# Kernel optimization log

Hardware: AMD Instinct MI355X
Metric: run time of the kernel (lower is better)

The kernel has to match this reference:

```python
import jax, jax.numpy as jnp
import numpy as np

N_NODES = 50000
N_EDGES = 800000
NUM_FEATURES = 3
HIDDEN = 128
NUM_GRAPHS = 100
NUM_CLASSES = 2


def setup_inputs() -> dict:
    key = jax.random.key(0)
    ks = jax.random.split(key, 12)
    x = jax.random.normal(ks[0], (N_NODES, NUM_FEATURES), dtype=jnp.float32)
    edge_index = jax.random.randint(ks[1], (2, N_EDGES), 0, N_NODES, dtype=jnp.int64)
    batch = jnp.sort(jax.random.randint(ks[2], (N_NODES,), 0, NUM_GRAPHS, dtype=jnp.int64))
    c1, c2, c3 = 4 * HIDDEN, 2 * HIDDEN, HIDDEN  # 512, 256, 128

    def glorot(k, fan_in, fan_out):
        s = jnp.sqrt(6.0 / (fan_in + fan_out)).astype(jnp.float32)
        return jax.random.uniform(k, (fan_in, fan_out), jnp.float32, -s, s)

    W1 = glorot(ks[3], NUM_FEATURES, c1); b1 = jnp.zeros((c1,), jnp.float32)
    W2 = glorot(ks[4], c1, c2);           b2 = jnp.zeros((c2,), jnp.float32)
    W3 = glorot(ks[5], c2, c3);           b3 = jnp.zeros((c3,), jnp.float32)
    Wc = glorot(ks[6], c3, NUM_CLASSES);  bc = jnp.zeros((NUM_CLASSES,), jnp.float32)
    return {"x": x, "W1": W1, "b1": b1, "W2": W2, "b2": b2, "W3": W3, "b3": b3,
            "Wc": Wc, "bc": bc, "edge_index": edge_index, "batch": batch}


def reference(x, W1, b1, W2, b2, W3, b3, Wc, bc, edge_index, batch):
    n = x.shape[0]
    self_loop = jnp.arange(n, dtype=edge_index.dtype)
    row = jnp.concatenate([edge_index[0], self_loop])  # source nodes (messages from)
    col = jnp.concatenate([edge_index[1], self_loop])  # target nodes (aggregate into)
    # symmetric GCN normalization with self-loops: deg^{-1/2}[row] * deg^{-1/2}[col]
    deg = jax.ops.segment_sum(jnp.ones(row.shape, x.dtype), col, num_segments=n)
    dis = jnp.where(deg > 0, jax.lax.rsqrt(jnp.maximum(deg, 1.0)), 0.0)
    norm = dis[row] * dis[col]  # [E + N]

    def gcn_conv(h, W, b):
        m = h @ W                                   # project first (cheap GEMM)
        agg = jax.ops.segment_sum(norm[:, None] * m[row], col, num_segments=n)
        return agg + b

    h = jax.nn.relu(gcn_conv(x, W1, b1))
    h = jax.nn.relu(gcn_conv(h, W2, b2))
    h = jax.nn.relu(gcn_conv(h, W3, b3))

    # global mean pool over graphs
    counts = jax.ops.segment_sum(jnp.ones((n,), h.dtype), batch, num_segments=NUM_GRAPHS)
    pooled = jax.ops.segment_sum(h, batch, num_segments=NUM_GRAPHS) / jnp.maximum(counts, 1.0)[:, None]

    logits = pooled @ Wc + bc
    return jax.nn.log_softmax(logits, axis=1)
```

## Files before the change

kernel.cpp:

```cpp
#include <hip/hip_runtime.h>
#include <hip/hip_bf16.h>
#include <hip/hip_fp8.h>
#include <math.h>

#define N_NODES 50000
#define N_EDGES 800000
#define NFEAT 3
#define C1 512
#define C2 256
#define C3 128
#define NGRAPH 100
#define NCLS 2
#define PSPLIT 8
#define NRANGE 8
#define RANGE_SZ 6250

typedef short bh8 __attribute__((ext_vector_type(8)));
typedef float f32x4 __attribute__((ext_vector_type(4)));

__device__ __forceinline__ short f2bf(float x) {
    __hip_bfloat16 h = __float2bfloat16(x);
    return *reinterpret_cast<short*>(&h);
}
__device__ __forceinline__ float bflo(unsigned int u) { return __uint_as_float(u << 16); }
__device__ __forceinline__ float bfhi(unsigned int u) { return __uint_as_float(u & 0xffff0000u); }
__device__ __forceinline__ unsigned int packbf(float a, float b) {
    return (unsigned int)(unsigned short)f2bf(a) | ((unsigned int)(unsigned short)f2bf(b) << 16);
}
__device__ __forceinline__ unsigned char f2fp8(float x) {
    __hip_fp8_e4m3 q(x);
    return (unsigned char)q.__x;
}
__device__ __forceinline__ float2 fp8x2(unsigned short u) {
    __hip_fp8x2_e4m3 q; q.__x = u; return (float2)q;
}


__global__ void count_edges(const int* __restrict__ col, int* __restrict__ counts) {
    int range = blockIdx.x & (NRANGE - 1);
    int e = (blockIdx.x >> 3) * 256 + threadIdx.x;
    if (e < N_EDGES) {
        int c = col[e];
        int lo = range * RANGE_SZ;
        if (c >= lo && c < lo + RANGE_SZ) atomicAdd(&counts[c], 1);
    }
}


__global__ void scan_chunks(const int* __restrict__ counts, const float* __restrict__ x,
                            int* __restrict__ offsets, int* __restrict__ chunksums,
                            float* __restrict__ dis, float4* __restrict__ xd) {
    __shared__ int s[256];
    int b = blockIdx.x, t = threadIdx.x;
    int i = b * 256 + t;
    int v = (i < N_NODES) ? counts[i] : 0;
    if (i < N_NODES) {
        float d = rsqrtf((float)(v + 1));
        dis[i] = d;
        xd[i] = make_float4(x[i * 3 + 0], x[i * 3 + 1], x[i * 3 + 2], d);
    }
    s[t] = v;
    __syncthreads();
    for (int d = 1; d < 256; d <<= 1) {
        int add = (t >= d) ? s[t - d] : 0;
        __syncthreads();
        s[t] += add;
        __syncthreads();
    }
    if (i < N_NODES) offsets[i + 1] = s[t];
    if (t == 255) chunksums[b] = s[255];
}

__global__ void scan_sums(int* __restrict__ chunksums, int nchunks) {
    __shared__ int s[256];
    int t = threadIdx.x;
    int v = (t < nchunks) ? chunksums[t] : 0;
    s[t] = v;
    __syncthreads();
    for (int d = 1; d < 256; d <<= 1) {
        int add = (t >= d) ? s[t - d] : 0;
        __syncthreads();
        s[t] += add;
        __syncthreads();
    }
    if (t < nchunks) chunksums[t] = (t == 0) ? 0 : s[t - 1];
}

__global__ void finalize_offsets(int* __restrict__ offsets, const int* __restrict__ chunkoffs,
                                 int* __restrict__ cursor) {
    int i = blockIdx.x * blockDim.x + threadIdx.x;
    if (i < N_NODES) {
        int v = offsets[i + 1] + chunkoffs[i / 256];
        offsets[i + 1] = v;
        if (i + 1 < N_NODES) cursor[i + 1] = v;
    }
    if (i == 0) { offsets[0] = 0; cursor[0] = 0; }
}

__global__ void scatter_edges(const int* __restrict__ rowi, const int* __restrict__ coli,
                              int* __restrict__ cursor, int* __restrict__ csr_src) {
    int range = blockIdx.x & (NRANGE - 1);
    int e = (blockIdx.x >> 3) * 256 + threadIdx.x;
    if (e < N_EDGES) {
        int c = coli[e];
        int lo = range * RANGE_SZ;
        if (c >= lo && c < lo + RANGE_SZ) {
            int p = atomicAdd(&cursor[c], 1);
            csr_src[p] = rowi[e];
        }
    }
}


__global__ void prep_weights(const float* __restrict__ W2, const float* __restrict__ W3,
                             short* __restrict__ W2t, short* __restrict__ W3t) {
    int idx = blockIdx.x * 256 + threadIdx.x;
    if (idx < C1 * C2) {
        int n = idx / C1, k = idx % C1;
        W2t[idx] = f2bf(W2[k * C2 + n]);
    } else if (idx < C1 * C2 + C2 * C3) {
        int j = idx - C1 * C2;
        int n = j / C2, k = j % C2;
        W3t[j] = f2bf(W3[k * C3 + n]);
    }
}


__global__ __launch_bounds__(256) void agg_feat3(const float4* __restrict__ xd,
                                                 const int* __restrict__ offsets,
                                                 const int* __restrict__ csr_src,
                                                 float* __restrict__ aggx) {
    int t = threadIdx.x;
    int l = t & 15;
    int i = blockIdx.x * 16 + (t >> 4);
    if (i >= N_NODES) return;
    int s = offsets[i], e = offsets[i + 1];
    float a0 = 0.f, a1 = 0.f, a2 = 0.f;
    for (int p = s + l; p < e; p += 16) {
        int r = csr_src[p];
        float4 v = xd[r];
        a0 += v.w * v.x;
        a1 += v.w * v.y;
        a2 += v.w * v.z;
    }
#pragma unroll
    for (int m = 1; m < 16; m <<= 1) {
        a0 += __shfl_xor(a0, m);
        a1 += __shfl_xor(a1, m);
        a2 += __shfl_xor(a2, m);
    }
    if (l == 0) {
        float4 self = xd[i];
        float di = self.w;
        a0 += di * self.x; a1 += di * self.y; a2 += di * self.z;
        aggx[i * 3 + 0] = di * a0;
        aggx[i * 3 + 1] = di * a1;
        aggx[i * 3 + 2] = di * a2;
    }
}


__global__ __launch_bounds__(512, 4) void gemm_l1(const float* __restrict__ aggx,
                                                  const float* __restrict__ W1,
                                                  const float* __restrict__ b1,
                                                  const float* __restrict__ dis,
                                                  const short* __restrict__ Bt,
                                                  unsigned char* __restrict__ Cmat, int M) {
    __shared__ short As[128 * 32];
    __shared__ short Bs[C2 * 32];
    __shared__ float sW1[3 * C1];
    __shared__ float sb1[C1];
    __shared__ float sa[128 * 3];
    __shared__ float sd[128];
    int bm = blockIdx.x * 128;
    int t = threadIdx.x;
    int wave = t >> 6, lane = t & 63, quad = lane >> 4, l16 = lane & 15;
    int wm = (wave >> 2) * 64;
    int wn = (wave & 3) * 64;
    f32x4 acc[4][4] = {};

    for (int j = t; j < 3 * C1; j += 512) sW1[j] = W1[j];
    if (t < C1) sb1[t] = b1[t];
    if (t < 128 * 3) {
        int r = bm + t / 3; if (r > M - 1) r = M - 1;
        sa[t] = aggx[r * 3 + (t % 3)];
    }
    if (t < 128) {
        int r = bm + t; if (r > M - 1) r = M - 1;
        sd[t] = dis[r];
    }
    __syncthreads();

    int ar = t >> 2, ak = (t & 3) * 8;
    int br = t >> 1, bk = (t & 1) * 16;
    float a0 = sa[ar * 3 + 0], a1 = sa[ar * 3 + 1], a2 = sa[ar * 3 + 2];
    float drow = sd[ar];

    for (int k0 = 0; k0 < C1; k0 += 32) {
#pragma unroll
        for (int j = 0; j < 8; ++j) {
            int k = k0 + ak + j;
            float v = a0 * sW1[k] + a1 * sW1[C1 + k] + a2 * sW1[2 * C1 + k] + sb1[k];
            As[ar * 32 + ak + j] = f2bf(drow * fmaxf(v, 0.f));
        }
        const short* bptr = Bt + (size_t)br * C1 + bk + k0;
        *(bh8*)&Bs[br * 32 + bk]     = *(const bh8*)bptr;
        *(bh8*)&Bs[br * 32 + bk + 8] = *(const bh8*)(bptr + 8);
        __syncthreads();
        bh8 af[4], bf[4];
#pragma unroll
        for (int mt = 0; mt < 4; ++mt)
            af[mt] = *(const bh8*)&As[(wm + mt * 16 + l16) * 32 + quad * 8];
#pragma unroll
        for (int nt = 0; nt < 4; ++nt)
            bf[nt] = *(const bh8*)&Bs[(wn + nt * 16 + l16) * 32 + quad * 8];
#pragma unroll
        for (int mt = 0; mt < 4; ++mt)
#pragma unroll
            for (int nt = 0; nt < 4; ++nt)
                acc[mt][nt] = __builtin_amdgcn_mfma_f32_16x16x32_bf16(af[mt], bf[nt], acc[mt][nt], 0, 0, 0);
        __syncthreads();
    }

#pragma unroll
    for (int mt = 0; mt < 4; ++mt)
#pragma unroll
        for (int nt = 0; nt < 4; ++nt) {
            int colc = wn + nt * 16 + l16;
#pragma unroll
            for (int r = 0; r < 4; ++r) {
                int rowc = bm + wm + mt * 16 + quad * 4 + r;
                if (rowc < M) Cmat[(size_t)rowc * C2 + colc] = f2fp8(acc[mt][nt][r]);
            }
        }
}


template <int K, int BN>
__global__ __launch_bounds__(512, 4) void gemm_bf16(const short* __restrict__ A,
                                                    const short* __restrict__ Bt,
                                                    unsigned char* __restrict__ Cmat, int M) {
    __shared__ short As[128 * 32];
    __shared__ short Bs[BN * 32];
    constexpr int NT = BN / 64;
    int bm = blockIdx.x * 128;
    int t = threadIdx.x;
    int wave = t >> 6, lane = t & 63, quad = lane >> 4, l16 = lane & 15;
    int wm = (wave >> 2) * 64;
    int wn = (wave & 3) * (BN / 4);
    f32x4 acc[4][NT] = {};

    int ar = t >> 2, ak = (t & 3) * 8;
    int agr = bm + ar; if (agr > M - 1) agr = M - 1;
    const short* aptr = A + (size_t)agr * K + ak;

    for (int k0 = 0; k0 < K; k0 += 32) {
        *(bh8*)&As[ar * 32 + ak] = *(const bh8*)(aptr + k0);
        if constexpr (BN == 256) {
            int br = t >> 1, bk = (t & 1) * 16;
            const short* bptr = Bt + (size_t)br * K + bk + k0;
            *(bh8*)&Bs[br * 32 + bk]     = *(const bh8*)bptr;
            *(bh8*)&Bs[br * 32 + bk + 8] = *(const bh8*)(bptr + 8);
        } else {
            int br = t >> 2, bk = (t & 3) * 8;
            *(bh8*)&Bs[br * 32 + bk] = *(const bh8*)(Bt + (size_t)br * K + bk + k0);
        }
        __syncthreads();
        bh8 af[4], bf[NT];
#pragma unroll
        for (int mt = 0; mt < 4; ++mt)
            af[mt] = *(const bh8*)&As[(wm + mt * 16 + l16) * 32 + quad * 8];
#pragma unroll
        for (int nt = 0; nt < NT; ++nt)
            bf[nt] = *(const bh8*)&Bs[(wn + nt * 16 + l16) * 32 + quad * 8];
#pragma unroll
        for (int mt = 0; mt < 4; ++mt)
#pragma unroll
            for (int nt = 0; nt < NT; ++nt)
                acc[mt][nt] = __builtin_amdgcn_mfma_f32_16x16x32_bf16(af[mt], bf[nt], acc[mt][nt], 0, 0, 0);
        __syncthreads();
    }

#pragma unroll
    for (int mt = 0; mt < 4; ++mt)
#pragma unroll
        for (int nt = 0; nt < NT; ++nt) {
            int colc = wn + nt * 16 + l16;
#pragma unroll
            for (int r = 0; r < 4; ++r) {
                int rowc = bm + wm + mt * 16 + quad * 4 + r;
                if (rowc < M) Cmat[(size_t)rowc * BN + colc] = f2fp8(acc[mt][nt][r]);
            }
        }
}


template <int C, bool PRESCALE>
__global__ void aggregate_ns(const unsigned char* __restrict__ m, const int* __restrict__ offsets,
                             const int* __restrict__ csr_src, const float* __restrict__ dis,
                             const float* __restrict__ bias, short* __restrict__ out) {
    int i = blockIdx.x;
    int t = threadIdx.x;
    float di = dis[i];
    const unsigned short* mu = (const unsigned short*)m;
    float2 sf = fp8x2(mu[(size_t)i * (C / 2) + t]);
    float acc0 = sf.x, acc1 = sf.y;
    int s = offsets[i], e = offsets[i + 1];
    int p = s;
    for (; p + 8 <= e; p += 8) {
        int r0 = csr_src[p],     r1 = csr_src[p + 1], r2 = csr_src[p + 2], r3 = csr_src[p + 3];
        int r4 = csr_src[p + 4], r5 = csr_src[p + 5], r6 = csr_src[p + 6], r7 = csr_src[p + 7];
        unsigned short u0 = mu[(size_t)r0 * (C / 2) + t];
        unsigned short u1 = mu[(size_t)r1 * (C / 2) + t];
        unsigned short u2 = mu[(size_t)r2 * (C / 2) + t];
        unsigned short u3 = mu[(size_t)r3 * (C / 2) + t];
        unsigned short u4 = mu[(size_t)r4 * (C / 2) + t];
        unsigned short u5 = mu[(size_t)r5 * (C / 2) + t];
        unsigned short u6 = mu[(size_t)r6 * (C / 2) + t];
        unsigned short u7 = mu[(size_t)r7 * (C / 2) + t];
        float2 f0 = fp8x2(u0), f1 = fp8x2(u1), f2 = fp8x2(u2), f3 = fp8x2(u3);
        float2 f4 = fp8x2(u4), f5 = fp8x2(u5), f6 = fp8x2(u6), f7 = fp8x2(u7);
        acc0 += f0.x + f1.x + f2.x + f3.x + f4.x + f5.x + f6.x + f7.x;
        acc1 += f0.y + f1.y + f2.y + f3.y + f4.y + f5.y + f6.y + f7.y;
    }
    for (; p < e; ++p) {
        int r = csr_src[p];
        float2 f = fp8x2(mu[(size_t)r * (C / 2) + t]);
        acc0 += f.x;
        acc1 += f.y;
    }
    acc0 = fmaxf(di * acc0 + bias[2 * t], 0.f);
    acc1 = fmaxf(di * acc1 + bias[2 * t + 1], 0.f);
    if (PRESCALE) { acc0 *= di; acc1 *= di; }
    ((unsigned int*)out)[(size_t)i * (C / 2) + t] = packbf(acc0, acc1);
}


__global__ void pool_partial(const short* __restrict__ h3, const int* __restrict__ batch,
                             float* __restrict__ pooled) {
    int g = blockIdx.x, sp = blockIdx.y;
    int t = threadIdx.x;
    __shared__ int seg[2];
    if (t < 2) {
        int target = g + t;
        int lo = 0, hi = N_NODES;
        while (lo < hi) { int mid = (lo + hi) >> 1; if (batch[mid] < target) lo = mid + 1; else hi = mid; }
        seg[t] = lo;
    }
    __syncthreads();
    int start = seg[0], end = seg[1];
    int len = end - start;
    int chunk = (len + PSPLIT - 1) / PSPLIT;
    int a = start + sp * chunk;
    int b = a + chunk; if (b > end) b = end;
    if (a >= b) return;
    const unsigned int* hu = (const unsigned int*)h3;
    float s0 = 0.f, s1 = 0.f;
    int i = a;
    for (; i + 4 <= b; i += 4) {
        unsigned int u0 = hu[(size_t)(i + 0) * (C3 / 2) + t];
        unsigned int u1 = hu[(size_t)(i + 1) * (C3 / 2) + t];
        unsigned int u2 = hu[(size_t)(i + 2) * (C3 / 2) + t];
        unsigned int u3 = hu[(size_t)(i + 3) * (C3 / 2) + t];
        s0 += bflo(u0) + bflo(u1) + bflo(u2) + bflo(u3);
        s1 += bfhi(u0) + bfhi(u1) + bfhi(u2) + bfhi(u3);
    }
    for (; i < b; ++i) {
        unsigned int u = hu[(size_t)i * (C3 / 2) + t];
        s0 += bflo(u);
        s1 += bfhi(u);
    }
    atomicAdd(&pooled[g * C3 + 2 * t], s0);
    atomicAdd(&pooled[g * C3 + 2 * t + 1], s1);
}


__global__ void finalize_head(const float* __restrict__ pooled, const int* __restrict__ batch,
                              const float* __restrict__ Wc, const float* __restrict__ bc,
                              float* __restrict__ outp) {
    int g = blockIdx.x;
    int t = threadIdx.x;
    __shared__ int seg[2];
    if (t < 2) {
        int target = g + t;
        int lo = 0, hi = N_NODES;
        while (lo < hi) { int mid = (lo + hi) >> 1; if (batch[mid] < target) lo = mid + 1; else hi = mid; }
        seg[t] = lo;
    }
    __syncthreads();
    float cnt = (float)(seg[1] - seg[0]);
    float pv = pooled[(size_t)g * C3 + t] / fmaxf(cnt, 1.f);
    float p0 = pv * Wc[t * 2 + 0];
    float p1 = pv * Wc[t * 2 + 1];
#pragma unroll
    for (int o = 32; o > 0; o >>= 1) {
        p0 += __shfl_down(p0, o);
        p1 += __shfl_down(p1, o);
    }
    __shared__ float r0[2], r1[2];
    int wid = t >> 6, lane = t & 63;
    if (lane == 0) { r0[wid] = p0; r1[wid] = p1; }
    __syncthreads();
    if (t == 0) {
        float l0 = r0[0] + r0[1] + bc[0];
        float l1 = r1[0] + r1[1] + bc[1];
        float mx = fmaxf(l0, l1);
        float lse = mx + logf(expf(l0 - mx) + expf(l1 - mx));
        outp[g * 2 + 0] = l0 - lse;
        outp[g * 2 + 1] = l1 - lse;
    }
}


extern "C" void kernel_launch(void* const* d_in, const int* in_sizes, int n_in,
                              void* d_out, int out_size, void* d_ws, size_t ws_size,
                              hipStream_t stream) {
    const float* x = (const float*)d_in[0];
    const float* W1 = (const float*)d_in[1];
    const float* b1 = (const float*)d_in[2];
    const float* W2 = (const float*)d_in[3];
    const float* b2 = (const float*)d_in[4];
    const float* W3 = (const float*)d_in[5];
    const float* b3 = (const float*)d_in[6];
    const float* Wc = (const float*)d_in[7];
    const float* bc = (const float*)d_in[8];
    const int* ei = (const int*)d_in[9];
    const int* batch = (const int*)d_in[10];
    const int* row = ei;
    const int* col = ei + N_EDGES;
    float* out = (float*)d_out;

    char* ws = (char*)d_ws;
    size_t off = 0;
    auto alloc = [&](size_t bytes) -> void* {
        off = (off + 255) & ~(size_t)255;
        void* p = ws + off;
        off += bytes;
        return p;
    };

    int* counts = (int*)alloc((size_t)N_NODES * 4);
    int* offsets = (int*)alloc((size_t)(N_NODES + 1) * 4);
    int* cursor = (int*)alloc((size_t)N_NODES * 4);
    int* chunksums = (int*)alloc(256 * 4);
    float* dis = (float*)alloc((size_t)N_NODES * 4);
    float4* xd = (float4*)alloc((size_t)N_NODES * 16);
    int* csr_src = (int*)alloc((size_t)N_EDGES * 4);
    float* aggx = (float*)alloc((size_t)N_NODES * 3 * 4);
    short* W2t = (short*)alloc((size_t)C1 * C2 * 2);
    short* W3t = (short*)alloc((size_t)C2 * C3 * 2);
    unsigned char* m2 = (unsigned char*)alloc((size_t)N_NODES * C2);
    short* h2 = (short*)alloc((size_t)N_NODES * C2 * 2);
    unsigned char* m3 = (unsigned char*)alloc((size_t)N_NODES * C3);
    short* h3 = (short*)alloc((size_t)N_NODES * C3 * 2);
    float* pooled = (float*)alloc((size_t)NGRAPH * C3 * 4);

    hipMemsetAsync(counts, 0, (size_t)N_NODES * 4, stream);
    hipMemsetAsync(pooled, 0, (size_t)NGRAPH * C3 * 4, stream);
    int nechunks = (N_EDGES + 255) / 256;
    count_edges<<<nechunks * NRANGE, 256, 0, stream>>>(col, counts);
    int nchunks = (N_NODES + 255) / 256;
    scan_chunks<<<nchunks, 256, 0, stream>>>(counts, x, offsets, chunksums, dis, xd);
    scan_sums<<<1, 256, 0, stream>>>(chunksums, nchunks);
    finalize_offsets<<<(N_NODES + 255) / 256, 256, 0, stream>>>(offsets, chunksums, cursor);
    scatter_edges<<<nechunks * NRANGE, 256, 0, stream>>>(row, col, cursor, csr_src);

    prep_weights<<<(C1 * C2 + C2 * C3 + 255) / 256, 256, 0, stream>>>(W2, W3, W2t, W3t);

    agg_feat3<<<(N_NODES + 15) / 16, 256, 0, stream>>>(xd, offsets, csr_src, aggx);

    gemm_l1<<<(N_NODES + 127) / 128, 512, 0, stream>>>(aggx, W1, b1, dis, W2t, m2, N_NODES);
    aggregate_ns<C2, true><<<N_NODES, C2 / 2, 0, stream>>>(m2, offsets, csr_src, dis, b2, h2);

    gemm_bf16<C2, C3><<<(N_NODES + 127) / 128, 512, 0, stream>>>(h2, W3t, m3, N_NODES);
    aggregate_ns<C3, false><<<N_NODES, C3 / 2, 0, stream>>>(m3, offsets, csr_src, dis, b3, h3);

    dim3 gp(NGRAPH, PSPLIT);
    pool_partial<<<gp, C3 / 2, 0, stream>>>(h3, batch, pooled);
    finalize_head<<<NGRAPH, C3, 0, stream>>>(pooled, batch, Wc, bc, out);
}
```

Baseline: 301.5 us.

## Aggregate with one wavefront per node, wider loads and deeper gather unroll

Replaces the per-node block aggregation with a kernel that packs four nodes per 256-thread block, one 64-lane wavefront per node. For C=256, each lane loads 4 fp8 values as a uint32. Node offsets and scale are made wave-uniform via readfirstlane, the gather is unrolled to 16 neighbours, and the tail is handled with a masked 16-wide batch. The aim is fewer tiny blocks, more memory-level parallelism per wave and wider loads. The cost is higher register pressure and some wasted tail loads.

```diff
diff --git a/kernel.cpp b/kernel.cpp
--- a/kernel.cpp
+++ b/kernel.cpp
@@ -296,43 +296,111 @@
 
 
 template <int C, bool PRESCALE>
-__global__ void aggregate_ns(const unsigned char* __restrict__ m, const int* __restrict__ offsets,
-                             const int* __restrict__ csr_src, const float* __restrict__ dis,
-                             const float* __restrict__ bias, short* __restrict__ out) {
-    int i = blockIdx.x;
-    int t = threadIdx.x;
-    float di = dis[i];
-    const unsigned short* mu = (const unsigned short*)m;
-    float2 sf = fp8x2(mu[(size_t)i * (C / 2) + t]);
-    float acc0 = sf.x, acc1 = sf.y;
-    int s = offsets[i], e = offsets[i + 1];
-    int p = s;
-    for (; p + 8 <= e; p += 8) {
-        int r0 = csr_src[p],     r1 = csr_src[p + 1], r2 = csr_src[p + 2], r3 = csr_src[p + 3];
-        int r4 = csr_src[p + 4], r5 = csr_src[p + 5], r6 = csr_src[p + 6], r7 = csr_src[p + 7];
-        unsigned short u0 = mu[(size_t)r0 * (C / 2) + t];
-        unsigned short u1 = mu[(size_t)r1 * (C / 2) + t];
-        unsigned short u2 = mu[(size_t)r2 * (C / 2) + t];
-        unsigned short u3 = mu[(size_t)r3 * (C / 2) + t];
-        unsigned short u4 = mu[(size_t)r4 * (C / 2) + t];
-        unsigned short u5 = mu[(size_t)r5 * (C / 2) + t];
-        unsigned short u6 = mu[(size_t)r6 * (C / 2) + t];
-        unsigned short u7 = mu[(size_t)r7 * (C / 2) + t];
-        float2 f0 = fp8x2(u0), f1 = fp8x2(u1), f2 = fp8x2(u2), f3 = fp8x2(u3);
-        float2 f4 = fp8x2(u4), f5 = fp8x2(u5), f6 = fp8x2(u6), f7 = fp8x2(u7);
-        acc0 += f0.x + f1.x + f2.x + f3.x + f4.x + f5.x + f6.x + f7.x;
-        acc1 += f0.y + f1.y + f2.y + f3.y + f4.y + f5.y + f6.y + f7.y;
-    }
-    for (; p < e; ++p) {
-        int r = csr_src[p];
-        float2 f = fp8x2(mu[(size_t)r * (C / 2) + t]);
-        acc0 += f.x;
-        acc1 += f.y;
-    }
-    acc0 = fmaxf(di * acc0 + bias[2 * t], 0.f);
-    acc1 = fmaxf(di * acc1 + bias[2 * t + 1], 0.f);
-    if (PRESCALE) { acc0 *= di; acc1 *= di; }
-    ((unsigned int*)out)[(size_t)i * (C / 2) + t] = packbf(acc0, acc1);
+__global__ __launch_bounds__(256) void aggregate_w(const unsigned char* __restrict__ m,
+                                                   const int* __restrict__ offsets,
+                                                   const int* __restrict__ csr_src,
+                                                   const float* __restrict__ dis,
+                                                   const float* __restrict__ bias,
+                                                   short* __restrict__ out) {
+    int i = blockIdx.x * 4 + (threadIdx.x >> 6);
+    if (i >= N_NODES) return;
+    int lane = threadIdx.x & 63;
+    int s = __builtin_amdgcn_readfirstlane(offsets[i]);
+    int e = __builtin_amdgcn_readfirstlane(offsets[i + 1]);
+    float di = __uint_as_float(__builtin_amdgcn_readfirstlane(__float_as_uint(dis[i])));
+
+    if constexpr (C == 256) {
+        const unsigned int* mu = (const unsigned int*)m;
+        unsigned int su = mu[(size_t)i * (C / 4) + lane];
+        float2 slo = fp8x2((unsigned short)(su & 0xffffu));
+        float2 shi = fp8x2((unsigned short)(su >> 16));
+        float a0 = slo.x, a1 = slo.y, a2 = shi.x, a3 = shi.y;
+        int p = s;
+        for (; p + 16 <= e; p += 16) {
+            unsigned int u[16];
+#pragma unroll
+            for (int j = 0; j < 16; ++j) {
+                int r = csr_src[p + j];
+                u[j] = mu[(size_t)r * (C / 4) + lane];
+            }
+#pragma unroll
+            for (int j = 0; j < 16; ++j) {
+                float2 lo = fp8x2((unsigned short)(u[j] & 0xffffu));
+                float2 hi = fp8x2((unsigned short)(u[j] >> 16));
+                a0 += lo.x; a1 += lo.y; a2 += hi.x; a3 += hi.y;
+            }
+        }
+        if (p < e) {
+            unsigned int u[16];
+            float sc[16];
+#pragma unroll
+            for (int j = 0; j < 16; ++j) {
+                int q = p + j;
+                sc[j] = (q < e) ? 1.f : 0.f;
+                int r = csr_src[(q < e) ? q : e - 1];
+                u[j] = mu[(size_t)r * (C / 4) + lane];
+            }
+#pragma unroll
+            for (int j = 0; j < 16; ++j) {
+                float2 lo = fp8x2((unsigned short)(u[j] & 0xffffu));
+                float2 hi = fp8x2((unsigned short)(u[j] >> 16));
+                a0 = fmaf(sc[j], lo.x, a0);
+                a1 = fmaf(sc[j], lo.y, a1);
+                a2 = fmaf(sc[j], hi.x, a2);
+                a3 = fmaf(sc[j], hi.y, a3);
+            }
+        }
+        float4 b = *(const float4*)&bias[4 * lane];
+        a0 = fmaxf(di * a0 + b.x, 0.f);
+        a1 = fmaxf(di * a1 + b.y, 0.f);
+        a2 = fmaxf(di * a2 + b.z, 0.f);
+        a3 = fmaxf(di * a3 + b.w, 0.f);
+        if (PRESCALE) { a0 *= di; a1 *= di; a2 *= di; a3 *= di; }
+        uint2 o;
+        o.x = packbf(a0, a1);
+        o.y = packbf(a2, a3);
+        *(uint2*)(out + (size_t)i * C + 4 * lane) = o;
+    } else {
+        const unsigned short* mu = (const unsigned short*)m;
+        float2 sf = fp8x2(mu[(size_t)i * (C / 2) + lane]);
+        float a0 = sf.x, a1 = sf.y;
+        int p = s;
+        for (; p + 16 <= e; p += 16) {
+            unsigned short u[16];
+#pragma unroll
+            for (int j = 0; j < 16; ++j) {
+                int r = csr_src[p + j];
+                u[j] = mu[(size_t)r * (C / 2) + lane];
+            }
+#pragma unroll
+            for (int j = 0; j < 16; ++j) {
+                float2 f = fp8x2(u[j]);
+                a0 += f.x; a1 += f.y;
+            }
+        }
+        if (p < e) {
+            unsigned short u[16];
+            float sc[16];
+#pragma unroll
+            for (int j = 0; j < 16; ++j) {
+                int q = p + j;
+                sc[j] = (q < e) ? 1.f : 0.f;
+                int r = csr_src[(q < e) ? q : e - 1];
+                u[j] = mu[(size_t)r * (C / 2) + lane];
+            }
+#pragma unroll
+            for (int j = 0; j < 16; ++j) {
+                float2 f = fp8x2(u[j]);
+                a0 = fmaf(sc[j], f.x, a0);
+                a1 = fmaf(sc[j], f.y, a1);
+            }
+        }
+        float2 b = *(const float2*)&bias[2 * lane];
+        a0 = fmaxf(di * a0 + b.x, 0.f);
+        a1 = fmaxf(di * a1 + b.y, 0.f);
+        if (PRESCALE) { a0 *= di; a1 *= di; }
+        ((unsigned int*)out)[(size_t)i * (C / 2) + lane] = packbf(a0, a1);
+    }
 }
 
 
@@ -470,10 +538,10 @@
     agg_feat3<<<(N_NODES + 15) / 16, 256, 0, stream>>>(xd, offsets, csr_src, aggx);
 
     gemm_l1<<<(N_NODES + 127) / 128, 512, 0, stream>>>(aggx, W1, b1, dis, W2t, m2, N_NODES);
-    aggregate_ns<C2, true><<<N_NODES, C2 / 2, 0, stream>>>(m2, offsets, csr_src, dis, b2, h2);
+    aggregate_w<C2, true><<<(N_NODES + 3) / 4, 256, 0, stream>>>(m2, offsets, csr_src, dis, b2, h2);
 
     gemm_bf16<C2, C3><<<(N_NODES + 127) / 128, 512, 0, stream>>>(h2, W3t, m3, N_NODES);
-    aggregate_ns<C3, false><<<N_NODES, C3 / 2, 0, stream>>>(m3, offsets, csr_src, dis, b3, h3);
+    aggregate_w<C3, false><<<(N_NODES + 3) / 4, 256, 0, stream>>>(m3, offsets, csr_src, dis, b3, h3);
 
     dim3 gp(NGRAPH, PSPLIT);
     pool_partial<<<gp, C3 / 2, 0, stream>>>(h3, batch, pooled);
```

Measured after the change: 282.9 us. -6.2%, faster.
